# Optimization experiments

Measured on AMD Instinct MI355X. Metric: run time of the kernel, lower is better.

The kernel has to match this reference:

```python
import jax, jax.numpy as jnp
import numpy as np

N, C, H, W = 2048, 16, 32, 32
E = 16384


def _conv(x, w, b):
    # 3x3 conv, stride 1, padding 1, NCHW/OIHW
    y = jax.lax.conv_general_dilated(
        x, w, window_strides=(1, 1), padding=((1, 1), (1, 1)),
        dimension_numbers=('NCHW', 'OIHW', 'NCHW'))
    return y + b[None, :, None, None]


def _get_nodes(fv, edges, positive):
    # fv: [N,C,H,W]; edges: [E,3] = (a, rel, b)
    rel = edges[:, 1]
    m = (rel > 0) if positive else (rel < 0)
    wmask = m.astype(fv.dtype)[:, None, None, None]  # [E,1,1,1]
    a = edges[:, 0]
    b = edges[:, 2]
    # symmetric scatter_add: fv[a] -> b and fv[b] -> a (masked edges contribute 0)
    nodes = jnp.zeros_like(fv)
    nodes = nodes.at[b].add(fv[a] * wmask)
    nodes = nodes.at[a].add(fv[b] * wmask)
    return nodes


def setup_inputs() -> dict:
    key = jax.random.key(0)
    ks = jax.random.split(key, 10)
    x = jax.random.normal(ks[0], (N, C, H, W), dtype=jnp.float32)
    ids = jax.random.randint(ks[1], (E, 2), 0, N)
    rel = jnp.where(jax.random.bernoulli(ks[2], 0.5, (E,)), 1, -1).astype(jnp.int64)
    edges = jnp.stack([ids[:, 0].astype(jnp.int64), rel, ids[:, 1].astype(jnp.int64)], axis=1)
    s = 0.05
    w1 = jax.random.normal(ks[3], (32, 48, 3, 3), dtype=jnp.float32) * s
    b1 = jax.random.normal(ks[4], (32,), dtype=jnp.float32) * s
    w2 = jax.random.normal(ks[5], (32, 32, 3, 3), dtype=jnp.float32) * s
    b2 = jax.random.normal(ks[6], (32,), dtype=jnp.float32) * s
    w3 = jax.random.normal(ks[7], (16, 32, 3, 3), dtype=jnp.float32) * s
    b3 = jax.random.normal(ks[8], (16,), dtype=jnp.float32) * s
    return {"x": x, "edges": edges, "w1": w1, "b1": b1, "w2": w2, "b2": b2, "w3": w3, "b3": b3}


def reference(x, edges, w1, b1, w2, b2, w3, b3):
    neigh = _get_nodes(x, edges, True)
    non_neigh = _get_nodes(x, edges, False)
    enc = jnp.concatenate([x, neigh, non_neigh], axis=1)  # [N,48,H,W]
    h = _conv(enc, w1, b1)
    h = _conv(h, w2, b2)
    return _conv(h, w3, b3)  # [N,16,H,W]
```

## Files before the change

### kernel.cpp

```cpp
#include <hip/hip_runtime.h>


#define NNODES 2048
#define HW 1024
#define PLANE 16384
#define CAP 128
#define SLICE_PX 32
#define NSLICE 32
#define NPB 8

typedef float v4f __attribute__((ext_vector_type(4)));
typedef short v8s __attribute__((ext_vector_type(8)));

__device__ inline unsigned short f2bfu(float f) {
    unsigned u = __float_as_uint(f);
    u += 0x7fffu + ((u >> 16) & 1u);
    return (unsigned short)(u >> 16);
}
__device__ inline unsigned pk2(float a, float b) {
    return (unsigned)f2bfu(a) | ((unsigned)f2bfu(b) << 16);
}
__device__ inline void add2(float& a, float& b, unsigned u) {
    a += __uint_as_float(u << 16);
    b += __uint_as_float(u & 0xffff0000u);
}

__global__ __launch_bounds__(256) void build_lists(
    const int* __restrict__ edges, int E, int* __restrict__ cnt, int* __restrict__ lists)
{
    int e = blockIdx.x * 256 + threadIdx.x;
    if (e >= E) return;
    int a = edges[3 * e + 0];
    int rel = edges[3 * e + 1];
    int b = edges[3 * e + 2];
    int s = (rel > 0) ? 0 : 1;
    int slot = atomicAdd(&cnt[b * 2 + s], 1);
    if (slot < CAP) lists[((size_t)(b * 2 + s)) * CAP + slot] = a;
    slot = atomicAdd(&cnt[a * 2 + s], 1);
    if (slot < CAP) lists[((size_t)(a * 2 + s)) * CAP + slot] = b;
}

__global__ __launch_bounds__(256) void xpose_bf16(
    const float* __restrict__ x, ushort* __restrict__ xb)
{
    int n = blockIdx.x, t = threadIdx.x;
    const float4* src = (const float4*)(x + (size_t)n * PLANE);
    float vv[64];
#pragma unroll
    for (int i = 0; i < 16; i++) {
        float4 v = src[i * 256 + t];
        vv[i * 4 + 0] = v.x; vv[i * 4 + 1] = v.y; vv[i * 4 + 2] = v.z; vv[i * 4 + 3] = v.w;
    }
    uint4* dst = (uint4*)(xb + (size_t)n * HW * 16);
#pragma unroll
    for (int j = 0; j < 4; j++) {
        uint4 o0, o1;
        o0.x = pk2(vv[0 * 4 + j], vv[1 * 4 + j]);
        o0.y = pk2(vv[2 * 4 + j], vv[3 * 4 + j]);
        o0.z = pk2(vv[4 * 4 + j], vv[5 * 4 + j]);
        o0.w = pk2(vv[6 * 4 + j], vv[7 * 4 + j]);
        o1.x = pk2(vv[8 * 4 + j], vv[9 * 4 + j]);
        o1.y = pk2(vv[10 * 4 + j], vv[11 * 4 + j]);
        o1.z = pk2(vv[12 * 4 + j], vv[13 * 4 + j]);
        o1.w = pk2(vv[14 * 4 + j], vv[15 * 4 + j]);
        dst[(4 * t + j) * 2 + 0] = o0;
        dst[(4 * t + j) * 2 + 1] = o1;
    }
}

__global__ __launch_bounds__(256) void gather_enc_slice(
    const ushort* __restrict__ xb, const int* __restrict__ cnt,
    const int* __restrict__ lists, ushort* __restrict__ enc)
{
    int idx = blockIdx.x;
    int x8 = idx & 7;
    int g  = (idx >> 3) & 255;
    int p  = idx >> 11;
    int slice = p * 8 + x8;
    int t = threadIdx.x;
    int node = g * NPB + (t >> 5);
    int px = slice * SLICE_PX + (t & 31);

    const uint4* xsrc = (const uint4*)(xb + ((size_t)node * HW + px) * 16);
    uint4* edst = (uint4*)(enc + ((size_t)node * HW + px) * 48);
    edst[0] = xsrc[0];
    edst[1] = xsrc[1];

    for (int s = 0; s < 2; s++) {
        int d = min(cnt[node * 2 + s], CAP);
        const int* lst = lists + (size_t)(node * 2 + s) * CAP;
        float acc[16];
#pragma unroll
        for (int i = 0; i < 16; i++) acc[i] = 0.f;
        int nb = (d > 0) ? lst[0] : 0;
        for (int k = 0; k < d; k++) {
            const uint4* sp = (const uint4*)(xb + ((size_t)nb * HW + px) * 16);
            uint4 p0 = sp[0];
            uint4 p1 = sp[1];
            nb = (k + 1 < d) ? lst[k + 1] : 0;
            add2(acc[0],  acc[1],  p0.x);
            add2(acc[2],  acc[3],  p0.y);
            add2(acc[4],  acc[5],  p0.z);
            add2(acc[6],  acc[7],  p0.w);
            add2(acc[8],  acc[9],  p1.x);
            add2(acc[10], acc[11], p1.y);
            add2(acc[12], acc[13], p1.z);
            add2(acc[14], acc[15], p1.w);
        }
        uint4 o0, o1;
        o0.x = pk2(acc[0],  acc[1]);  o0.y = pk2(acc[2],  acc[3]);
        o0.z = pk2(acc[4],  acc[5]);  o0.w = pk2(acc[6],  acc[7]);
        o1.x = pk2(acc[8],  acc[9]);  o1.y = pk2(acc[10], acc[11]);
        o1.z = pk2(acc[12], acc[13]); o1.w = pk2(acc[14], acc[15]);
        edst[2 + s * 2 + 0] = o0;
        edst[2 + s * 2 + 1] = o1;
    }
}

template<int CI_REAL, int KCH, int CO>
__global__ __launch_bounds__(256) void prep_wfrag(
    const float* __restrict__ wt, ushort* __restrict__ wf)
{
    const int total = (CO / 16) * 9 * KCH * 64;
    for (int idx = blockIdx.x * 256 + threadIdx.x; idx < total; idx += gridDim.x * 256) {
        int lane = idx & 63;
        int t = idx >> 6;
        int kc = t % KCH; t /= KCH;
        int khw = t % 9;  t /= 9;
        int cot = t;
        int nco = cot * 16 + (lane & 15);
        int kq  = lane >> 4;
        float w[8];
#pragma unroll
        for (int j = 0; j < 8; j++) {
            int k = kc * 32 + kq * 8 + j;
            w[j] = (k < CI_REAL) ? wt[((size_t)nco * CI_REAL + k) * 9 + khw] : 0.f;
        }
        uint4 o;
        o.x = pk2(w[0], w[1]); o.y = pk2(w[2], w[3]);
        o.z = pk2(w[4], w[5]); o.w = pk2(w[6], w[7]);
        *(uint4*)&wf[(size_t)idx * 8] = o;
    }
}

template<int CI_REAL, int CIP_G, int CIP_L, int KCH, int CO, bool OUT_F32>
__global__ __launch_bounds__(256) void conv_mfma(
    const ushort* __restrict__ in, const ushort* __restrict__ wf,
    const float* __restrict__ bias, ushort* __restrict__ outb,
    float* __restrict__ outf)
{
    __shared__ ushort tile[320 * CIP_L + 8];
    const int n = blockIdx.x >> 2;
    const int r0 = (blockIdx.x & 3) * 8;
    const int CH4 = CIP_G / 8;

    const uint4* gsrc = (const uint4*)(in + (size_t)n * HW * CIP_G);
    for (int idx = threadIdx.x; idx < 320 * CH4; idx += 256) {
        int lp = idx / CH4;
        int ch = idx - lp * CH4;
        int gr = r0 - 1 + (lp >> 5);
        uint4 val = make_uint4(0, 0, 0, 0);
        if (gr >= 0 && gr < 32) val = gsrc[(size_t)(gr * 32 + (lp & 31)) * CH4 + ch];
        *(uint4*)&tile[lp * CIP_L + ch * 8] = val;
    }
    __syncthreads();

    const int wv = threadIdx.x >> 6;
    const int lane = threadIdx.x & 63;
    const int l15 = lane & 15;
    const int kq = lane >> 4;

    const int cotile = (CO == 32) ? (wv >> 1) : 0;
    const int cob = cotile * 16;
    const int nco = cob + l15;

    const v8s* wfv = (const v8s*)wf;
    v8s bfrag[9 * KCH];
#pragma unroll
    for (int khw = 0; khw < 9; khw++)
#pragma unroll
        for (int kc = 0; kc < KCH; kc++)
            bfrag[khw * KCH + kc] = wfv[(size_t)(((cotile * 9 + khw) * KCH + kc) * 64 + lane)];
    const float bv = bias[nco];

    int mt0, mtstep, nmt;
    if (CO == 32) { mt0 = wv & 1; mtstep = 2; nmt = 8; }
    else          { mt0 = wv;     mtstep = 4; nmt = 4; }

    for (int it = 0; it < nmt; it++) {
        int mtile = mt0 + it * mtstep;
        int r = r0 + (mtile >> 1);
        int c = (mtile & 1) * 16 + l15;
        v4f acc = {bv, bv, bv, bv};
#pragma unroll
        for (int khw = 0; khw < 9; khw++) {
            int dh = khw / 3 - 1, dw = (khw % 3) - 1;
            int rr = r + dh;
            if (rr < 0 || rr > 31) continue;
            int cc = c + dw;
            bool okc = (cc >= 0) && (cc <= 31);
            int lp = (rr - r0 + 1) * 32 + (okc ? cc : 0);
#pragma unroll
            for (int kc = 0; kc < KCH; kc++) {
                v8s a = *(const v8s*)&tile[lp * CIP_L + kc * 32 + kq * 8];
                bool kok = (kc * 32 + 32 <= CI_REAL) || (kc * 32 + kq * 8 < CI_REAL);
                if (!okc || !kok) a = (v8s)0;
                acc = __builtin_amdgcn_mfma_f32_16x16x32_bf16(a, bfrag[khw * KCH + kc], acc, 0, 0, 0);
            }
        }
        int pbase = r * 32 + (mtile & 1) * 16 + kq * 4;
        if (OUT_F32) {
            float4 o; o.x = acc[0]; o.y = acc[1]; o.z = acc[2]; o.w = acc[3];
            *(float4*)(outf + ((size_t)n * CO + nco) * HW + pbase) = o;
        } else {
#pragma unroll
            for (int reg = 0; reg < 4; reg++)
                outb[((size_t)n * HW + pbase + reg) * CO + nco] = (ushort)f2bfu(acc[reg]);
        }
    }
}

extern "C" void kernel_launch(void* const* d_in, const int* in_sizes, int n_in,
                              void* d_out, int out_size, void* d_ws, size_t ws_size,
                              hipStream_t stream)
{
    const float* x     = (const float*)d_in[0];
    const int*   edges = (const int*)d_in[1];
    const float* w1    = (const float*)d_in[2];
    const float* b1    = (const float*)d_in[3];
    const float* w2    = (const float*)d_in[4];
    const float* b2    = (const float*)d_in[5];
    const float* w3    = (const float*)d_in[6];
    const float* b3    = (const float*)d_in[7];
    float* out = (float*)d_out;

    const int E = in_sizes[1] / 3;

    ushort* enc = (ushort*)d_ws;
    ushort* h1  = enc + (size_t)NNODES * HW * 48;
    ushort* xb  = h1  + (size_t)NNODES * HW * 32;
    int*    cnt   = (int*)(xb + (size_t)NNODES * HW * 16);
    int*    lists = cnt + NNODES * 2;
    ushort* wf1 = (ushort*)(lists + (size_t)NNODES * 2 * CAP);
    ushort* wf2 = wf1 + 2 * 9 * 2 * 64 * 8;
    ushort* wf3 = wf2 + 2 * 9 * 1 * 64 * 8;
    ushort* h2  = enc;

    hipMemsetAsync(cnt, 0, NNODES * 2 * sizeof(int), stream);
    build_lists<<<(E + 255) / 256, 256, 0, stream>>>(edges, E, cnt, lists);

    prep_wfrag<48, 2, 32><<<9, 256, 0, stream>>>(w1, wf1);
    prep_wfrag<32, 1, 32><<<5, 256, 0, stream>>>(w2, wf2);
    prep_wfrag<32, 1, 16><<<3, 256, 0, stream>>>(w3, wf3);

    xpose_bf16<<<NNODES, 256, 0, stream>>>(x, xb);
    gather_enc_slice<<<NSLICE * (NNODES / NPB), 256, 0, stream>>>(xb, cnt, lists, enc);

    conv_mfma<48, 48, 56, 2, 32, false><<<NNODES * 4, 256, 0, stream>>>(enc, wf1, b1, h1, nullptr);
    conv_mfma<32, 32, 40, 1, 32, false><<<NNODES * 4, 256, 0, stream>>>(h1, wf2, b2, h2, nullptr);
    conv_mfma<32, 32, 40, 1, 16, true><<<NNODES * 4, 256, 0, stream>>>(h2, wf3, b3, nullptr, out);
}
```

Baseline: 694.5 us.

## Stop copying x into enc; conv1 reads x channels directly from xb

The gather kernel no longer copies the bf16 x channels into the 48-channel enc buffer. enc now holds only the 32 neighbour channels, and the first conv loads its first 16 channels straight from xb through a second input pointer. The gather kernel also stages each block's adjacency lists and degrees in shared memory, software-pipelines the neighbour loads two deep, and writes its output with nontemporal stores. This removes a redundant write and read of x and cuts scattered global list reads, in exchange for a slightly more complex, branchier conv tile load.

```diff
diff --git a/kernel.cpp b/kernel.cpp
--- a/kernel.cpp
+++ b/kernel.cpp
@@ -11,6 +11,7 @@
 
 typedef float v4f __attribute__((ext_vector_type(4)));
 typedef short v8s __attribute__((ext_vector_type(8)));
+typedef unsigned int v4u __attribute__((ext_vector_type(4)));
 
 __device__ inline unsigned short f2bfu(float f) {
     unsigned u = __float_as_uint(f);
@@ -68,6 +69,12 @@
     }
 }
 
+#define ACC16(P0, P1) do { \
+    add2(acc[0],  acc[1],  (P0).x); add2(acc[2],  acc[3],  (P0).y); \
+    add2(acc[4],  acc[5],  (P0).z); add2(acc[6],  acc[7],  (P0).w); \
+    add2(acc[8],  acc[9],  (P1).x); add2(acc[10], acc[11], (P1).y); \
+    add2(acc[12], acc[13], (P1).z); add2(acc[14], acc[15], (P1).w); } while (0)
+
 __global__ __launch_bounds__(256) void gather_enc_slice(
     const ushort* __restrict__ xb, const int* __restrict__ cnt,
     const int* __restrict__ lists, ushort* __restrict__ enc)
@@ -78,42 +85,53 @@
     int p  = idx >> 11;
     int slice = p * 8 + x8;
     int t = threadIdx.x;
-    int node = g * NPB + (t >> 5);
+    int nodebase = g * NPB;
+    int node = nodebase + (t >> 5);
     int px = slice * SLICE_PX + (t & 31);
 
-    const uint4* xsrc = (const uint4*)(xb + ((size_t)node * HW + px) * 16);
-    uint4* edst = (uint4*)(enc + ((size_t)node * HW + px) * 48);
-    edst[0] = xsrc[0];
-    edst[1] = xsrc[1];
-
+    __shared__ int slist[NPB * 2 * CAP];
+    __shared__ int sdeg[NPB * 2];
+    {
+        const uint4* lsrc = (const uint4*)(lists + (size_t)nodebase * 2 * CAP);
+        uint4* ldst = (uint4*)slist;
+        ldst[t] = lsrc[t];
+        ldst[256 + t] = lsrc[256 + t];
+        if (t < NPB * 2) sdeg[t] = min(cnt[nodebase * 2 + t], CAP);
+    }
+    __syncthreads();
+
+    v4u* edst = (v4u*)(enc + ((size_t)node * HW + px) * 32);
+#pragma unroll
     for (int s = 0; s < 2; s++) {
-        int d = min(cnt[node * 2 + s], CAP);
-        const int* lst = lists + (size_t)(node * 2 + s) * CAP;
+        const int lbase = ((t >> 5) * 2 + s) * CAP;
+        const int d = sdeg[(t >> 5) * 2 + s];
         float acc[16];
 #pragma unroll
         for (int i = 0; i < 16; i++) acc[i] = 0.f;
-        int nb = (d > 0) ? lst[0] : 0;
-        for (int k = 0; k < d; k++) {
-            const uint4* sp = (const uint4*)(xb + ((size_t)nb * HW + px) * 16);
-            uint4 p0 = sp[0];
-            uint4 p1 = sp[1];
-            nb = (k + 1 < d) ? lst[k + 1] : 0;
-            add2(acc[0],  acc[1],  p0.x);
-            add2(acc[2],  acc[3],  p0.y);
-            add2(acc[4],  acc[5],  p0.z);
-            add2(acc[6],  acc[7],  p0.w);
-            add2(acc[8],  acc[9],  p1.x);
-            add2(acc[10], acc[11], p1.y);
-            add2(acc[12], acc[13], p1.z);
-            add2(acc[14], acc[15], p1.w);
-        }
-        uint4 o0, o1;
+        v4u a0 = {0,0,0,0}, a1 = {0,0,0,0}, b0 = {0,0,0,0}, b1 = {0,0,0,0};
+        if (d >= 1) {
+            const v4u* sp = (const v4u*)(xb + ((size_t)slist[lbase] * HW + px) * 16);
+            a0 = sp[0]; a1 = sp[1];
+        }
+        if (d >= 2) {
+            const v4u* sp = (const v4u*)(xb + ((size_t)slist[lbase + 1] * HW + px) * 16);
+            b0 = sp[0]; b1 = sp[1];
+        }
+        for (int k = 2; k < d; k++) {
+            const v4u* sp = (const v4u*)(xb + ((size_t)slist[lbase + k] * HW + px) * 16);
+            v4u n0 = sp[0], n1 = sp[1];
+            ACC16(a0, a1);
+            a0 = b0; a1 = b1; b0 = n0; b1 = n1;
+        }
+        if (d >= 1) { ACC16(a0, a1); ACC16(b0, b1); }
+
+        v4u o0, o1;
         o0.x = pk2(acc[0],  acc[1]);  o0.y = pk2(acc[2],  acc[3]);
         o0.z = pk2(acc[4],  acc[5]);  o0.w = pk2(acc[6],  acc[7]);
         o1.x = pk2(acc[8],  acc[9]);  o1.y = pk2(acc[10], acc[11]);
         o1.z = pk2(acc[12], acc[13]); o1.w = pk2(acc[14], acc[15]);
-        edst[2 + s * 2 + 0] = o0;
-        edst[2 + s * 2 + 1] = o1;
+        __builtin_nontemporal_store(o0, edst + s * 2 + 0);
+        __builtin_nontemporal_store(o1, edst + s * 2 + 1);
     }
 }
 
@@ -143,24 +161,30 @@
     }
 }
 
-template<int CI_REAL, int CIP_G, int CIP_L, int KCH, int CO, bool OUT_F32>
+template<int CI_REAL, int CIP_G, int CIP_L, int KCH, int CO, bool OUT_F32, bool SPLIT>
 __global__ __launch_bounds__(256) void conv_mfma(
-    const ushort* __restrict__ in, const ushort* __restrict__ wf,
-    const float* __restrict__ bias, ushort* __restrict__ outb,
-    float* __restrict__ outf)
+    const ushort* __restrict__ in, const ushort* __restrict__ in2,
+    const ushort* __restrict__ wf, const float* __restrict__ bias,
+    ushort* __restrict__ outb, float* __restrict__ outf)
 {
     __shared__ ushort tile[320 * CIP_L + 8];
     const int n = blockIdx.x >> 2;
     const int r0 = (blockIdx.x & 3) * 8;
     const int CH4 = CIP_G / 8;
-
-    const uint4* gsrc = (const uint4*)(in + (size_t)n * HW * CIP_G);
+    const int CH4_1 = SPLIT ? (CH4 - 2) : CH4;
+
+    const uint4* gsrc  = (const uint4*)(in + (size_t)n * HW * (CH4_1 * 8));
+    const uint4* gsrc2 = SPLIT ? (const uint4*)(in2 + (size_t)n * HW * 16) : nullptr;
     for (int idx = threadIdx.x; idx < 320 * CH4; idx += 256) {
         int lp = idx / CH4;
         int ch = idx - lp * CH4;
         int gr = r0 - 1 + (lp >> 5);
         uint4 val = make_uint4(0, 0, 0, 0);
-        if (gr >= 0 && gr < 32) val = gsrc[(size_t)(gr * 32 + (lp & 31)) * CH4 + ch];
+        if (gr >= 0 && gr < 32) {
+            size_t gpx = (size_t)(gr * 32 + (lp & 31));
+            if (SPLIT && ch < 2) val = gsrc2[gpx * 2 + ch];
+            else                 val = gsrc[gpx * CH4_1 + (SPLIT ? ch - 2 : ch)];
+        }
         *(uint4*)&tile[lp * CIP_L + ch * 8] = val;
     }
     __syncthreads();
@@ -237,7 +261,7 @@
     const int E = in_sizes[1] / 3;
 
     ushort* enc = (ushort*)d_ws;
-    ushort* h1  = enc + (size_t)NNODES * HW * 48;
+    ushort* h1  = enc + (size_t)NNODES * HW * 32;
     ushort* xb  = h1  + (size_t)NNODES * HW * 32;
     int*    cnt   = (int*)(xb + (size_t)NNODES * HW * 16);
     int*    lists = cnt + NNODES * 2;
@@ -256,7 +280,7 @@
     xpose_bf16<<<NNODES, 256, 0, stream>>>(x, xb);
     gather_enc_slice<<<NSLICE * (NNODES / NPB), 256, 0, stream>>>(xb, cnt, lists, enc);
 
-    conv_mfma<48, 48, 56, 2, 32, false><<<NNODES * 4, 256, 0, stream>>>(enc, wf1, b1, h1, nullptr);
-    conv_mfma<32, 32, 40, 1, 32, false><<<NNODES * 4, 256, 0, stream>>>(h1, wf2, b2, h2, nullptr);
-    conv_mfma<32, 32, 40, 1, 16, true><<<NNODES * 4, 256, 0, stream>>>(h2, wf3, b3, nullptr, out);
-}
+    conv_mfma<48, 48, 56, 2, 32, false, true><<<NNODES * 4, 256, 0, stream>>>(enc, xb, wf1, b1, h1, nullptr);
+    conv_mfma<32, 32, 40, 1, 32, false, false><<<NNODES * 4, 256, 0, stream>>>(h1, nullptr, wf2, b2, h2, nullptr);
+    conv_mfma<32, 32, 40, 1, 16, true, false><<<NNODES * 4, 256, 0, stream>>>(h2, nullptr, wf3, b3, nullptr, out);
+}
```

New measurement: 721.5 us. 1.04x slower.
